# Kernel optimization log

Hardware: AMD Instinct MI355X
Metric: run time of the kernel (lower is better)

## Reference

```python
import jax, jax.numpy as jnp
from jax import lax
import numpy as np
from jax.scipy.ndimage import map_coordinates

SIGMA = 1.0
RADIUS = 3          # from radius=(3,3); kernel size 7
TAU = (2.0, 2.0)
SCALE_FACTORS = (0.5, 1.0)
ITERATIONS = (2, 2)  # production uses (100,100); reduced for tractable reference
EPS = 1e-9
IN_EPS = 1e-5


def gaussian_kernel1d(sigma, radius):
    x = jnp.arange(-radius, radius + 1, dtype=jnp.float32)
    k = jnp.exp(-0.5 * (x / sigma) ** 2)
    return k / jnp.sum(k)


def smooth3d(vf, k):
    # separable depthwise Gaussian over the 3 spatial axes, SAME padding
    C = vf.shape[1]
    for ax in range(3):
        shp = [1, 1, 1]
        shp[ax] = k.shape[0]
        w = jnp.tile(k.reshape(1, 1, *shp), (C, 1, 1, 1, 1))
        vf = lax.conv_general_dilated(vf, w, (1, 1, 1), 'SAME',
                                      dimension_numbers=('NCDHW', 'OIDHW', 'NCDHW'),
                                      feature_group_count=C)
    return vf


def warp(img, vf):
    # img: [1,1,D,H,W], vf: [1,3,D,H,W] displacement in voxel units
    D, H, W = img.shape[2:]
    gz, gy, gx = jnp.meshgrid(jnp.arange(D, dtype=img.dtype),
                              jnp.arange(H, dtype=img.dtype),
                              jnp.arange(W, dtype=img.dtype), indexing='ij')
    coords = [gz + vf[0, 0], gy + vf[0, 1], gx + vf[0, 2]]
    out = map_coordinates(img[0, 0], coords, order=1, mode='nearest')
    return out[None, None]


def demon_forces(warped, fixed, spacing):
    # active demons: gradient of the (warped) moving image
    diff = warped - fixed  # [1,1,D,H,W]
    g = jnp.stack(jnp.gradient(warped[0, 0]), axis=0)[None]  # [1,3,D,H,W]
    g = g / spacing[None, :, None, None, None]
    denom = jnp.sum(g * g, axis=1, keepdims=True) + diff * diff
    return jnp.where(denom > EPS, diff * g / denom, 0.0)


def match_vf(vf, shape):
    # resize displacement field and rescale its magnitude per axis
    old = vf.shape[2:]
    if tuple(old) == tuple(shape):
        return vf
    scale = jnp.array([s1 / s2 for s1, s2 in zip(shape, old)], jnp.float32)
    vf = jax.image.resize(vf, vf.shape[:2] + tuple(shape), method='trilinear')
    return vf * scale[None, :, None, None, None]


def conv3d(x, w):
    return lax.conv_general_dilated(x, w, (1, 1, 1), 'SAME',
                                    dimension_numbers=('NCDHW', 'OIDHW', 'NCDHW'))


def instance_norm(x):
    m = jnp.mean(x, axis=(2, 3, 4), keepdims=True)
    v = jnp.var(x, axis=(2, 3, 4), keepdims=True)
    return (x - m) / jnp.sqrt(v + IN_EPS)


def mish(x):
    return x * jnp.tanh(jax.nn.softplus(x))


def setup_inputs() -> dict:
    key = jax.random.key(0)
    ks = jax.random.split(key, 8)
    D = 96
    image = jax.random.normal(ks[0], (1, 1, D, D, D), jnp.float32)
    moving = jax.random.normal(ks[1], (1, 1, D, D, D), jnp.float32)
    mask = jnp.ones((1, 1, D, D, D), jnp.float32)
    spacing = jnp.ones((3,), jnp.float32)
    w1 = jax.random.normal(ks[2], (32, 5, 3, 3, 3), jnp.float32) * 0.05
    w2 = jax.random.normal(ks[3], (64, 32, 3, 3, 3), jnp.float32) * 0.05
    w3 = jax.random.normal(ks[4], (32, 64, 3, 3, 3), jnp.float32) * 0.05
    w4 = jax.random.normal(ks[5], (3, 32, 3, 3, 3), jnp.float32) * 0.05
    b4 = jnp.zeros((3,), jnp.float32)
    return {'image': image, 'mask': mask, 'moving': moving, 'spacing': spacing,
            'w1': w1, 'w2': w2, 'w3': w3, 'w4': w4, 'b4': b4}


def reference(image, mask, moving, spacing, w1, w2, w3, w4, b4):
    kernel = gaussian_kernel1d(SIGMA, RADIUS)
    full_shape = image.shape[2:]
    vf = None
    for lvl, (sf, n_it) in enumerate(zip(SCALE_FACTORS, ITERATIONS)):
        shp = tuple(int(s * sf) for s in full_shape)
        f = jax.image.resize(image, image.shape[:2] + shp, method='trilinear')
        m = jax.image.resize(mask, mask.shape[:2] + shp, method='nearest')
        mv = jax.image.resize(moving, moving.shape[:2] + shp, method='trilinear')
        if vf is None:
            vf = jnp.zeros((image.shape[0], 3) + shp, jnp.float32)
        else:
            vf = match_vf(vf, shp)
        tau = TAU[lvl]

        def body(i, vf, mv=mv, f=f, m=m, tau=tau):
            warped = warp(mv, vf)
            vf = vf + tau * demon_forces(warped, f, spacing) * m
            return smooth3d(vf, kernel)

        vf = lax.fori_loop(0, n_it, body, vf)

    # the iterative registration runs under torch.no_grad()
    vf = lax.stop_gradient(vf)
    warped_moving = lax.stop_gradient(warp(moving, vf))  # last level is full scale

    # correction CNN: Conv3d/InstanceNorm3d/Mish stack on [vf, image*mask, warped_moving]
    x = jnp.concatenate([vf, image * mask, warped_moving], axis=1)  # [1,5,D,H,W]
    x = mish(instance_norm(conv3d(x, w1)))
    x = mish(instance_norm(conv3d(x, w2)))
    x = mish(instance_norm(conv3d(x, w3)))
    correction = conv3d(x, w4) + b4[None, :, None, None, None]
    corrected_vf = smooth3d(vf + correction, kernel)

    vf = match_vf(vf, full_shape)
    corrected_vf = match_vf(corrected_vf, full_shape)
    corrected_warped_moving = warp(moving, corrected_vf)
    return corrected_warped_moving, corrected_vf, vf
```

## Files before the change

### kernel.cpp

```cpp
#include <hip/hip_runtime.h>
#include <hip/hip_bf16.h>
#include <math.h>

#define DEV __device__ __forceinline__

constexpr int D96 = 96;
constexpr int N96 = D96 * D96 * D96;
constexpr int D48 = 48;
constexpr int N48 = D48 * D48 * D48;

#define GW0 0.3990502796524549f
#define GW1 0.2420362293761143f
#define GW2 0.05400558262251696f
#define GW3 0.004433048175243745f

typedef __attribute__((ext_vector_type(8))) short s16x8;
typedef __attribute__((ext_vector_type(4))) short s16x4;
typedef __attribute__((ext_vector_type(4))) float f32x4;
typedef __attribute__((ext_vector_type(16))) float f32x16;

DEV int clampi(int v, int lo, int hi) { return v < lo ? lo : (v > hi ? hi : v); }

DEV short f2bf(float f) { __hip_bfloat16 h = __float2bfloat16(f); short s; __builtin_memcpy(&s, &h, 2); return s; }
DEV float bf2f(short s) { __hip_bfloat16 h; __builtin_memcpy(&h, &s, 2); return __bfloat162float(h); }

__global__ void k_downsample2x(const float* __restrict__ src, float* __restrict__ dst)
{
    int idx = blockIdx.x * blockDim.x + threadIdx.x;
    if (idx >= N48) return;
    int x = idx % D48, y = (idx / D48) % D48, z = idx / (D48 * D48);

    float wz[4], wy[4], wx[4];
    int jz[4], jy[4], jx[4];
    auto mk = [](int i, float* w, int* j) {
        const float base[4] = {0.125f, 0.375f, 0.375f, 0.125f};
        float s = 0.f;
        #pragma unroll
        for (int t = 0; t < 4; ++t) {
            int jj = 2 * i - 1 + t;
            bool v = (jj >= 0) && (jj < D96);
            j[t] = v ? jj : 0;
            w[t] = v ? base[t] : 0.f;
            s += w[t];
        }
        float inv = 1.f / s;
        #pragma unroll
        for (int t = 0; t < 4; ++t) w[t] *= inv;
    };
    mk(z, wz, jz); mk(y, wy, jy); mk(x, wx, jx);

    float acc = 0.f;
    #pragma unroll
    for (int a = 0; a < 4; ++a) {
        #pragma unroll
        for (int b = 0; b < 4; ++b) {
            float wab = wz[a] * wy[b];
            int rowoff = (jz[a] * D96 + jy[b]) * D96;
            #pragma unroll
            for (int c = 0; c < 4; ++c)
                acc += wab * wx[c] * src[rowoff + jx[c]];
        }
    }
    dst[idx] = acc;
}

__global__ void k_upsample_vf(const float* __restrict__ src, float* __restrict__ dst)
{
    int idx = blockIdx.x * blockDim.x + threadIdx.x;
    if (idx >= 3 * N96) return;
    int c = idx / N96;
    int s = idx - c * N96;
    int x = s % D96, y = (s / D96) % D96, z = s / (D96 * D96);

    auto mk = [](int i, int* j, float* w) {
        int k = i >> 1;
        if ((i & 1) == 0) { j[0] = k - 1; w[0] = 0.25f; j[1] = k; w[1] = 0.75f; }
        else              { j[0] = k;     w[0] = 0.75f; j[1] = k + 1; w[1] = 0.25f; }
        float sum = 0.f;
        #pragma unroll
        for (int t = 0; t < 2; ++t) {
            bool v = (j[t] >= 0) && (j[t] < D48);
            if (!v) { w[t] = 0.f; j[t] = 0; }
            sum += w[t];
        }
        float inv = 1.f / sum;
        w[0] *= inv; w[1] *= inv;
    };
    int jz[2], jy[2], jx[2]; float wz[2], wy[2], wx[2];
    mk(z, jz, wz); mk(y, jy, wy); mk(x, jx, wx);

    const float* p = src + (size_t)c * N48;
    float acc = 0.f;
    #pragma unroll
    for (int a = 0; a < 2; ++a)
        #pragma unroll
        for (int b = 0; b < 2; ++b) {
            float wab = wz[a] * wy[b];
            int rowoff = (jz[a] * D48 + jy[b]) * D48;
            acc += wab * (wx[0] * p[rowoff + jx[0]] + wx[1] * p[rowoff + jx[1]]);
        }
    dst[idx] = 2.f * acc;
}

__global__ void k_warp(const float* __restrict__ img, const float* __restrict__ vf,
                       float* __restrict__ out, int D)
{
    int N = D * D * D;
    int idx = blockIdx.x * blockDim.x + threadIdx.x;
    if (idx >= N) return;
    int x = idx % D, y = (idx / D) % D, z = idx / (D * D);
    float cz = z + vf[idx], cy = y + vf[N + idx], cx = x + vf[2 * N + idx];
    float fz = floorf(cz), fy = floorf(cy), fx = floorf(cx);
    float wz = cz - fz, wy = cy - fy, wx = cx - fx;
    int z0 = clampi((int)fz, 0, D - 1), z1 = clampi((int)fz + 1, 0, D - 1);
    int y0 = clampi((int)fy, 0, D - 1), y1 = clampi((int)fy + 1, 0, D - 1);
    int x0 = clampi((int)fx, 0, D - 1), x1 = clampi((int)fx + 1, 0, D - 1);
    float v000 = img[(z0 * D + y0) * D + x0], v001 = img[(z0 * D + y0) * D + x1];
    float v010 = img[(z0 * D + y1) * D + x0], v011 = img[(z0 * D + y1) * D + x1];
    float v100 = img[(z1 * D + y0) * D + x0], v101 = img[(z1 * D + y0) * D + x1];
    float v110 = img[(z1 * D + y1) * D + x0], v111 = img[(z1 * D + y1) * D + x1];
    float c00 = v000 + wx * (v001 - v000);
    float c01 = v010 + wx * (v011 - v010);
    float c10 = v100 + wx * (v101 - v100);
    float c11 = v110 + wx * (v111 - v110);
    float c0 = c00 + wy * (c01 - c00);
    float c1 = c10 + wy * (c11 - c10);
    out[idx] = c0 + wz * (c1 - c0);
}

__global__ void k_forces(const float* __restrict__ warped, const float* __restrict__ fixed,
                         const float* __restrict__ mask, const float* __restrict__ spacing,
                         float* __restrict__ vf, int D, int maskD, float tau)
{
    int N = D * D * D;
    int idx = blockIdx.x * blockDim.x + threadIdx.x;
    if (idx >= N) return;
    int x = idx % D, y = (idx / D) % D, z = idx / (D * D);
    float w0 = warped[idx];
    float diff = w0 - fixed[idx];
    int sZ = D * D, sY = D;
    float gz = (z == 0) ? warped[idx + sZ] - w0 : (z == D - 1) ? w0 - warped[idx - sZ]
               : 0.5f * (warped[idx + sZ] - warped[idx - sZ]);
    float gy = (y == 0) ? warped[idx + sY] - w0 : (y == D - 1) ? w0 - warped[idx - sY]
               : 0.5f * (warped[idx + sY] - warped[idx - sY]);
    float gx = (x == 0) ? warped[idx + 1] - w0 : (x == D - 1) ? w0 - warped[idx - 1]
               : 0.5f * (warped[idx + 1] - warped[idx - 1]);
    gz /= spacing[0]; gy /= spacing[1]; gx /= spacing[2];
    float denom = gz * gz + gy * gy + gx * gx + diff * diff;
    float m;
    if (D == maskD) m = mask[idx];
    else {
        float r = (float)maskD / (float)D;
        int mz = clampi((int)((z + 0.5f) * r), 0, maskD - 1);
        int my = clampi((int)((y + 0.5f) * r), 0, maskD - 1);
        int mx = clampi((int)((x + 0.5f) * r), 0, maskD - 1);
        m = mask[(mz * maskD + my) * maskD + mx];
    }
    if (denom > 1e-9f) {
        float sc = tau * diff / denom * m;
        vf[idx]         += sc * gz;
        vf[N + idx]     += sc * gy;
        vf[2 * N + idx] += sc * gx;
    }
}

__global__ __launch_bounds__(256, 2)
void k_smooth3(const float* __restrict__ src, float* __restrict__ dst, int D)
{
    __shared__ float B1[10648];
    __shared__ float B2[7744];
    float* B3 = B1;
    int nt = D >> 4;
    int b = blockIdx.x;
    int tx = b % nt, ty = (b / nt) % nt, tz = b / (nt * nt);
    int c = blockIdx.y;
    int N = D * D * D;
    const float* s = src + (size_t)c * N;
    float* d = dst + (size_t)c * N;
    int x0 = tx * 16, y0 = ty * 16, z0 = tz * 16;
    int tid = threadIdx.x;

    for (int l = tid; l < 10648; l += 256) {
        int xx = l % 22, yy = (l / 22) % 22, zz = l / 484;
        int gz = z0 + zz - 3, gy = y0 + yy - 3, gx = x0 + xx - 3;
        float v = 0.f;
        if ((unsigned)gz < (unsigned)D && (unsigned)gy < (unsigned)D && (unsigned)gx < (unsigned)D)
            v = s[((size_t)gz * D + gy) * D + gx];
        B1[l] = v;
    }
    __syncthreads();
    for (int l = tid; l < 16 * 484; l += 256) {
        int xx = l % 22, yy = (l / 22) % 22, zo = l / 484;
        int base = (zo + 3) * 484 + yy * 22 + xx;
        B2[l] = GW0 * B1[base]
              + GW1 * (B1[base - 484] + B1[base + 484])
              + GW2 * (B1[base - 968] + B1[base + 968])
              + GW3 * (B1[base - 1452] + B1[base + 1452]);
    }
    __syncthreads();
    for (int l = tid; l < 16 * 16 * 22; l += 256) {
        int xx = l % 22, yo = (l / 22) % 16, zo = l / 352;
        int base = zo * 484 + (yo + 3) * 22 + xx;
        B3[l] = GW0 * B2[base]
              + GW1 * (B2[base - 22] + B2[base + 22])
              + GW2 * (B2[base - 44] + B2[base + 44])
              + GW3 * (B2[base - 66] + B2[base + 66]);
    }
    __syncthreads();
    for (int l = tid; l < 4096; l += 256) {
        int xo = l % 16, yo = (l / 16) % 16, zo = l / 256;
        int base = zo * 352 + yo * 22 + xo + 3;
        float a = GW0 * B3[base]
                + GW1 * (B3[base - 1] + B3[base + 1])
                + GW2 * (B3[base - 2] + B3[base + 2])
                + GW3 * (B3[base - 3] + B3[base + 3]);
        d[((size_t)(z0 + zo) * D + (y0 + yo)) * D + (x0 + xo)] = a;
    }
}

__global__ void k_pack_cl(const float* __restrict__ vf, const float* __restrict__ image,
                          const float* __restrict__ mask, const float* __restrict__ warped,
                          short* __restrict__ xin8)
{
    int i = blockIdx.x * blockDim.x + threadIdx.x;
    if (i >= N96) return;
    s16x8 v;
    v[0] = f2bf(vf[i]); v[1] = f2bf(vf[N96 + i]); v[2] = f2bf(vf[2 * N96 + i]);
    v[3] = f2bf(image[i] * mask[i]); v[4] = f2bf(warped[i]);
    v[5] = 0; v[6] = 0; v[7] = 0;
    *reinterpret_cast<s16x8*>(&xin8[(size_t)i * 8]) = v;
}

__global__ void k_wreorder_all(const float* __restrict__ w1, const float* __restrict__ w2,
                               const float* __restrict__ w3, const float* __restrict__ w4,
                               short* __restrict__ r1, short* __restrict__ r2,
                               short* __restrict__ r3, short* __restrict__ r4)
{
    int i = blockIdx.x * 256 + threadIdx.x;
    const int S1 = 7168, S2 = 55296, S3 = 55296, S4 = 13824;
    const float* w; short* r; int CIN, CINP, COUT, COUTP;
    int idx = i;
    if (idx < S1)              { w = w1; r = r1; CIN = 5;  CINP = 8;  COUT = 32; COUTP = 32; }
    else if ((idx -= S1) < S2) { w = w2; r = r2; CIN = 32; CINP = 32; COUT = 64; COUTP = 64; }
    else if ((idx -= S2) < S3) { w = w3; r = r3; CIN = 64; CINP = 64; COUT = 32; COUTP = 32; }
    else if ((idx -= S3) < S4) { w = w4; r = r4; CIN = 32; CINP = 32; COUT = 3;  COUTP = 16; }
    else return;
    int j = idx & 7;
    int co = (idx >> 3) % COUTP;
    int kg = idx / (8 * COUTP);
    int k = kg * 8 + j;
    int off = k / CINP, ci = k % CINP;
    float v = 0.f;
    if (co < COUT && off < 27 && ci < CIN)
        v = w[((size_t)co * CIN + ci) * 27 + off];
    r[idx] = f2bf(v);
}

DEV float mishf(float f)
{
    float e = __expf(f);
    float t = 1.f + e;
    float u = t * t + 1.f;
    return f - 2.f * f * __builtin_amdgcn_rcpf(u);
}

__global__ __launch_bounds__(256, 4)
void k_conv1(const short* __restrict__ act, const short* __restrict__ Wr,
             short* __restrict__ outcl, float* __restrict__ part)
{
    constexpr int YH = 6, TN = 3, KS = 14;
    constexpr int TILE_G = 3 * YH * 98;
    __shared__ __align__(16) short tile[TILE_G * 8];
    float* red = (float*)tile;

    int b = blockIdx.x;
    int xcd = b & 7, bidx = b >> 3;
    int zblk = xcd * 12 + bidx / 24;
    int y0 = (bidx % 24) * 4;

    int tid = threadIdx.x;
    int lane = tid & 63, wave = tid >> 6;
    int ln31 = lane & 31, hi = lane >> 5;

    for (int i = tid; i < TILE_G; i += 256) {
        int xi = i % 98, yi = (i / 98) % YH, zi = i / (98 * YH);
        int gz = zblk + zi - 1, gy = y0 + yi - 1, gx = xi - 1;
        s16x8 v = {0, 0, 0, 0, 0, 0, 0, 0};
        if ((unsigned)gz < 96u && (unsigned)gy < 96u && (unsigned)gx < 96u)
            v = *reinterpret_cast<const s16x8*>(&act[(size_t)((gz * 96 + gy) * 96 + gx) * 8]);
        *reinterpret_cast<s16x8*>(&tile[i * 8]) = v;
    }
    __syncthreads();

    f32x16 acc[TN];
    #pragma unroll
    for (int i = 0; i < TN; ++i)
        #pragma unroll
        for (int e = 0; e < 16; ++e) acc[i][e] = 0.f;

    int xb_[TN];
    #pragma unroll
    for (int i = 0; i < TN; ++i) xb_[i] = i * 32 + ln31;

    #pragma unroll
    for (int ks = 0; ks < KS; ++ks) {
        s16x8 a = *reinterpret_cast<const s16x8*>(&Wr[((size_t)(ks * 2 + hi) * 32 + ln31) * 8]);
        int off = ks * 2 + hi; if (off > 26) off = 26;
        int dz = off / 9, r9 = off - dz * 9, dy = r9 / 3, dx = r9 - dy * 3;
        #pragma unroll
        for (int i = 0; i < TN; ++i) {
            int gi = (dz * YH + wave + dy) * 98 + xb_[i] + dx;
            s16x8 bf = *reinterpret_cast<const s16x8*>(&tile[gi * 8]);
            acc[i] = __builtin_amdgcn_mfma_f32_32x32x16_bf16(a, bf, acc[i], 0, 0, 0);
        }
    }

    float st_s[16], st_q[16];
    #pragma unroll
    for (int j = 0; j < 16; ++j) { st_s[j] = 0.f; st_q[j] = 0.f; }
    #pragma unroll
    for (int i = 0; i < TN; ++i)
        #pragma unroll
        for (int e = 0; e < 16; ++e) {
            float v = acc[i][e];
            st_s[e] += v; st_q[e] += v * v;
        }
    #pragma unroll
    for (int j = 0; j < 16; ++j) {
        #pragma unroll
        for (int o = 1; o <= 16; o <<= 1) {
            st_s[j] += __shfl_xor(st_s[j], o);
            st_q[j] += __shfl_xor(st_q[j], o);
        }
    }

    __syncthreads();
    #pragma unroll
    for (int i = 0; i < TN; ++i) {
        int x = xb_[i];
        #pragma unroll
        for (int q = 0; q < 4; ++q) {
            s16x4 pk;
            #pragma unroll
            for (int r = 0; r < 4; ++r) pk[r] = f2bf(acc[i][q * 4 + r]);
            int bo = (((wave * 96 + x) * 32 + q * 8 + hi * 4) * 2) ^ ((x & 3) << 4);
            *reinterpret_cast<s16x4*>((char*)tile + bo) = pk;
        }
    }
    __syncthreads();
    for (int t = tid; t < 4 * 96 * 4; t += 256) {
        int gran = t & 3;
        int x = (t >> 2) % 96;
        int row = t / (4 * 96);
        int bo = (((row * 96 + x) * 32) * 2 + gran * 16) ^ ((x & 3) << 4);
        s16x8 v = *reinterpret_cast<const s16x8*>((char*)tile + bo);
        int vox = ((zblk * 96) + y0 + row) * 96 + x;
        *reinterpret_cast<s16x8*>(&outcl[(size_t)vox * 32 + gran * 8]) = v;
    }

    __syncthreads();
    if (ln31 == 0) {
        int base = (wave * 2 + hi) * 16;
        #pragma unroll
        for (int j = 0; j < 16; ++j) {
            red[(base + j) * 2]     = st_s[j];
            red[(base + j) * 2 + 1] = st_q[j];
        }
    }
    __syncthreads();
    if (tid < 64) {
        int c = tid >> 1, sel = tid & 1;
        int q = (c >> 3) & 3, hic = (c >> 2) & 1, r = c & 3;
        int j = q * 4 + r;
        float v = 0.f;
        #pragma unroll
        for (int w = 0; w < 4; ++w)
            v += red[((w * 2 + hic) * 16 + j) * 2 + sel];
        part[((size_t)c * gridDim.x + blockIdx.x) * 2 + sel] = v;
    }
}

__global__ __launch_bounds__(256, 4)
void k_conv_c2(const short* __restrict__ act, const short* __restrict__ Wr,
               short* __restrict__ outcl, float* __restrict__ part)
{
    constexpr int TN = 3, YH = 6;
    __shared__ __align__(16) short tile[YH * 98 * 32];
    float* red = (float*)tile;

    int bb = blockIdx.x;
    int xcd = bb & 7;
    int ch = (bb >> 3) & 1;
    int idx = bb >> 4;
    int zblk = xcd * 12 + idx / 24;
    int y0 = (idx % 24) * 4;
    int tileid = xcd * 288 + idx;

    int tid = threadIdx.x;
    int lane = tid & 63, wave = tid >> 6;
    int ln31 = lane & 31, hi = lane >> 5;

    int xb_[TN];
    #pragma unroll
    for (int i = 0; i < TN; ++i) xb_[i] = i * 32 + ln31;

    int baddr[TN][3][2];
    #pragma unroll
    for (int i = 0; i < TN; ++i)
        #pragma unroll
        for (int dx = 0; dx < 3; ++dx) {
            int xi = xb_[i] + dx;
            int sw = (xi >> 1) & 3;
            #pragma unroll
            for (int gs = 0; gs < 2; ++gs)
                baddr[i][dx][gs] = ((wave * 98 + xi) * 4 + ((gs * 2 + hi) ^ sw)) * 16;
        }

    f32x16 acc[TN];
    #pragma unroll
    for (int i = 0; i < TN; ++i)
        #pragma unroll
        for (int e = 0; e < 16; ++e) acc[i][e] = 0.f;

    for (int p = 0; p < 3; ++p) {
        int gz = zblk + p - 1;
        __syncthreads();
        #pragma unroll
        for (int it = 0; it < 5; ++it) {
            int i = it * 256 + tid;
            if (i < 1176) {
                int g2 = i & 1, x2 = i >> 1;
                int xi = x2 % 98, yi = x2 / 98;
                int gy = y0 + yi - 1, gx = xi - 1;
                s16x8 v0 = {0, 0, 0, 0, 0, 0, 0, 0}, v1 = v0;
                if ((unsigned)gz < 96u && (unsigned)gy < 96u && (unsigned)gx < 96u) {
                    const short* sp = &act[(size_t)((gz * 96 + gy) * 96 + gx) * 32 + g2 * 16];
                    v0 = *reinterpret_cast<const s16x8*>(sp);
                    v1 = *reinterpret_cast<const s16x8*>(sp + 8);
                }
                int s0 = (g2 * 2) ^ ((xi >> 1) & 3);
                short* dp = &tile[((yi * 98 + xi) << 2) * 8];
                *reinterpret_cast<s16x8*>(&dp[s0 * 8]) = v0;
                *reinterpret_cast<s16x8*>(&dp[(s0 ^ 1) * 8]) = v1;
            }
        }
        __syncthreads();
        int kgbase = p * 36;
        #pragma unroll
        for (int ks = 0; ks < 18; ++ks) {
            constexpr int offt[18] = {0,0,1,1,2,2,3,3,4,4,5,5,6,6,7,7,8,8};
            const int off = offt[ks], gs = ks & 1;
            int kg = kgbase + off * 4 + gs * 2 + hi;
            s16x8 A = *reinterpret_cast<const s16x8*>(
                &Wr[((size_t)kg * 64 + ch * 32 + ln31) * 8]);
            const int dy = off / 3, dx = off % 3;
            #pragma unroll
            for (int i = 0; i < TN; ++i) {
                s16x8 bf = *reinterpret_cast<const s16x8*>(
                    (const char*)tile + baddr[i][dx][gs] + dy * 6272);
                acc[i] = __builtin_amdgcn_mfma_f32_32x32x16_bf16(A, bf, acc[i], 0, 0, 0);
            }
        }
    }

    float st_s[16], st_q[16];
    #pragma unroll
    for (int j = 0; j < 16; ++j) { st_s[j] = 0.f; st_q[j] = 0.f; }
    #pragma unroll
    for (int i = 0; i < TN; ++i)
        #pragma unroll
        for (int e = 0; e < 16; ++e) {
            float v = acc[i][e];
            st_s[e] += v; st_q[e] += v * v;
        }
    #pragma unroll
    for (int j = 0; j < 16; ++j) {
        #pragma unroll
        for (int o = 1; o <= 16; o <<= 1) {
            st_s[j] += __shfl_xor(st_s[j], o);
            st_q[j] += __shfl_xor(st_q[j], o);
        }
    }

    __syncthreads();
    #pragma unroll
    for (int i = 0; i < TN; ++i) {
        int x = xb_[i];
        #pragma unroll
        for (int q = 0; q < 4; ++q) {
            s16x4 pk;
            #pragma unroll
            for (int r = 0; r < 4; ++r) pk[r] = f2bf(acc[i][q * 4 + r]);
            int bo = (((wave * 96 + x) * 32 + q * 8 + hi * 4) * 2) ^ ((x & 3) << 4);
            *reinterpret_cast<s16x4*>((char*)tile + bo) = pk;
        }
    }
    __syncthreads();
    for (int t = tid; t < 4 * 96 * 4; t += 256) {
        int gran = t & 3;
        int x = (t >> 2) % 96;
        int row = t / (4 * 96);
        int bo = (((row * 96 + x) * 32) * 2 + gran * 16) ^ ((x & 3) << 4);
        s16x8 v = *reinterpret_cast<const s16x8*>((char*)tile + bo);
        int vox = ((zblk * 96) + y0 + row) * 96 + x;
        *reinterpret_cast<s16x8*>(&outcl[(size_t)vox * 64 + ch * 32 + gran * 8]) = v;
    }

    __syncthreads();
    if (ln31 == 0) {
        int base = (wave * 2 + hi) * 16;
        #pragma unroll
        for (int j = 0; j < 16; ++j) {
            red[(base + j) * 2]     = st_s[j];
            red[(base + j) * 2 + 1] = st_q[j];
        }
    }
    __syncthreads();
    if (tid < 64) {
        int c = tid >> 1, sel = tid & 1;
        int q = (c >> 3) & 3, hic = (c >> 2) & 1, r = c & 3;
        int j = q * 4 + r;
        float v = 0.f;
        #pragma unroll
        for (int w = 0; w < 4; ++w)
            v += red[((w * 2 + hic) * 16 + j) * 2 + sel];
        part[((size_t)(ch * 32 + c) * 2304 + tileid) * 2 + sel] = v;
    }
}

__global__ __launch_bounds__(256, 4)
void k_conv_c3(const short* __restrict__ act, const short* __restrict__ Wr,
               short* __restrict__ outcl, float* __restrict__ part)
{
    constexpr int YH = 6;
    __shared__ __align__(16) short tile[YH * 98 * 32];
    float* red = (float*)tile;

    int bb = blockIdx.x;
    int xcd = bb & 7;
    int ch = (bb >> 3) & 1;
    int idx = bb >> 4;
    int zblk = xcd * 12 + idx / 24;
    int y0 = (idx % 24) * 4;
    int tileid = xcd * 288 + idx;

    int tid = threadIdx.x;
    int lane = tid & 63, wave = tid >> 6;
    int ln15 = lane & 15, lg = lane >> 4;

    int baddr[6][3];
    #pragma unroll
    for (int i = 0; i < 6; ++i)
        #pragma unroll
        for (int dx = 0; dx < 3; ++dx) {
            int xi = i * 16 + ln15 + dx;
            baddr[i][dx] = ((wave * 98 + xi) * 4 + (lg ^ ((xi >> 1) & 3))) * 16;
        }

    f32x4 acc[6];
    #pragma unroll
    for (int i = 0; i < 6; ++i) acc[i] = {0.f, 0.f, 0.f, 0.f};

    for (int p = 0; p < 3; ++p) {
        int gz = zblk + p - 1;
        for (int h = 0; h < 2; ++h) {
            __syncthreads();
            #pragma unroll
            for (int it = 0; it < 5; ++it) {
                int i = it * 256 + tid;
                if (i < 1176) {
                    int g2 = i & 1, x2 = i >> 1;
                    int xi = x2 % 98, yi = x2 / 98;
                    int gy = y0 + yi - 1, gx = xi - 1;
                    s16x8 v0 = {0, 0, 0, 0, 0, 0, 0, 0}, v1 = v0;
                    if ((unsigned)gz < 96u && (unsigned)gy < 96u && (unsigned)gx < 96u) {
                        const short* sp = &act[(size_t)((gz * 96 + gy) * 96 + gx) * 64
                                               + (h * 4 + g2 * 2) * 8];
                        v0 = *reinterpret_cast<const s16x8*>(sp);
                        v1 = *reinterpret_cast<const s16x8*>(sp + 8);
                    }
                    int s0 = (g2 * 2) ^ ((xi >> 1) & 3);
                    short* dp = &tile[((yi * 98 + xi) << 2) * 8];
                    *reinterpret_cast<s16x8*>(&dp[s0 * 8]) = v0;
                    *reinterpret_cast<s16x8*>(&dp[(s0 ^ 1) * 8]) = v1;
                }
            }
            __syncthreads();
            #pragma unroll
            for (int off = 0; off < 9; ++off) {
                int kg = (p * 9 + off) * 8 + h * 4 + lg;
                s16x8 A = *reinterpret_cast<const s16x8*>(
                    &Wr[((size_t)kg * 32 + ch * 16 + ln15) * 8]);
                const int dy = off / 3, dx = off % 3;
                #pragma unroll
                for (int i = 0; i < 6; ++i) {
                    s16x8 bf = *reinterpret_cast<const s16x8*>(
                        (const char*)tile + baddr[i][dx] + dy * 6272);
                    acc[i] = __builtin_amdgcn_mfma_f32_16x16x32_bf16(A, bf, acc[i], 0, 0, 0);
                }
            }
        }
    }

    float st_s[4], st_q[4];
    #pragma unroll
    for (int j = 0; j < 4; ++j) { st_s[j] = 0.f; st_q[j] = 0.f; }
    #pragma unroll
    for (int i = 0; i < 6; ++i)
        #pragma unroll
        for (int r = 0; r < 4; ++r) {
            float v = acc[i][r];
            st_s[r] += v; st_q[r] += v * v;
        }
    #pragma unroll
    for (int j = 0; j < 4; ++j) {
        #pragma unroll
        for (int o = 1; o <= 8; o <<= 1) {
            st_s[j] += __shfl_xor(st_s[j], o);
            st_q[j] += __shfl_xor(st_q[j], o);
        }
    }

    __syncthreads();
    #pragma unroll
    for (int i = 0; i < 6; ++i) {
        int x = i * 16 + ln15;
        s16x4 pk;
        #pragma unroll
        for (int r = 0; r < 4; ++r) pk[r] = f2bf(acc[i][r]);
        int bo = (((wave * 96 + x) * 16 + lg * 4) * 2) ^ ((x & 3) << 4);
        *reinterpret_cast<s16x4*>((char*)tile + bo) = pk;
    }
    __syncthreads();
    for (int t = tid; t < 4 * 96 * 2; t += 256) {
        int gran = t & 1;
        int x = (t >> 1) % 96;
        int row = t / (2 * 96);
        int bo = (((row * 96 + x) * 16) * 2 + gran * 16) ^ ((x & 3) << 4);
        s16x8 v = *reinterpret_cast<const s16x8*>((char*)tile + bo);
        int vox = ((zblk * 96) + y0 + row) * 96 + x;
        *reinterpret_cast<s16x8*>(&outcl[(size_t)vox * 32 + ch * 16 + gran * 8]) = v;
    }

    __syncthreads();
    if (ln15 == 0) {
        int base = (wave * 4 + lg) * 4;
        #pragma unroll
        for (int j = 0; j < 4; ++j) {
            red[(base + j) * 2]     = st_s[j];
            red[(base + j) * 2 + 1] = st_q[j];
        }
    }
    __syncthreads();
    if (tid < 32) {
        int c = tid >> 1, sel = tid & 1;
        float v = 0.f;
        #pragma unroll
        for (int w = 0; w < 4; ++w)
            v += red[((w * 4 + (c >> 2)) * 4 + (c & 3)) * 2 + sel];
        part[((size_t)(ch * 16 + c) * 2304 + tileid) * 2 + sel] = v;
    }
}

__global__ __launch_bounds__(256, 4)
void k_conv4(const short* __restrict__ act, const short* __restrict__ Wr,
             const float* __restrict__ bias, const float* __restrict__ vf,
             float* __restrict__ corr, float* __restrict__ outvf)
{
    constexpr int YH = 6;
    __shared__ __align__(16) short tile[YH * 98 * 32];

    int b = blockIdx.x;
    int xcd = b & 7, bidx = b >> 3;
    int zblk = xcd * 12 + bidx / 24;
    int y0 = (bidx % 24) * 4;

    int tid = threadIdx.x;
    int lane = tid & 63, wave = tid >> 6;
    int ln15 = lane & 15, lg = lane >> 4;

    int baddr[6][3];
    #pragma unroll
    for (int i = 0; i < 6; ++i)
        #pragma unroll
        for (int dx = 0; dx < 3; ++dx) {
            int xi = i * 16 + ln15 + dx;
            baddr[i][dx] = ((wave * 98 + xi) * 4 + (lg ^ ((xi >> 1) & 3))) * 16;
        }

    f32x4 acc[6];
    #pragma unroll
    for (int i = 0; i < 6; ++i) acc[i] = {0.f, 0.f, 0.f, 0.f};

    for (int p = 0; p < 3; ++p) {
        int gz = zblk + p - 1;
        __syncthreads();
        #pragma unroll
        for (int it = 0; it < 5; ++it) {
            int i = it * 256 + tid;
            if (i < 1176) {
                int g2 = i & 1, x2 = i >> 1;
                int xi = x2 % 98, yi = x2 / 98;
                int gy = y0 + yi - 1, gx = xi - 1;
                s16x8 v0 = {0, 0, 0, 0, 0, 0, 0, 0}, v1 = v0;
                if ((unsigned)gz < 96u && (unsigned)gy < 96u && (unsigned)gx < 96u) {
                    const short* sp = &act[(size_t)((gz * 96 + gy) * 96 + gx) * 32 + g2 * 16];
                    v0 = *reinterpret_cast<const s16x8*>(sp);
                    v1 = *reinterpret_cast<const s16x8*>(sp + 8);
                }
                int s0 = (g2 * 2) ^ ((xi >> 1) & 3);
                short* dp = &tile[((yi * 98 + xi) << 2) * 8];
                *reinterpret_cast<s16x8*>(&dp[s0 * 8]) = v0;
                *reinterpret_cast<s16x8*>(&dp[(s0 ^ 1) * 8]) = v1;
            }
        }
        __syncthreads();
        #pragma unroll
        for (int ks = 0; ks < 9; ++ks) {
            int kg = (p * 9 + ks) * 4 + lg;
            s16x8 a = *reinterpret_cast<const s16x8*>(&Wr[((size_t)kg * 16 + ln15) * 8]);
            const int dy = ks / 3, dx = ks % 3;
            #pragma unroll
            for (int i = 0; i < 6; ++i) {
                s16x8 bf = *reinterpret_cast<const s16x8*>(
                    (const char*)tile + baddr[i][dx] + dy * 6272);
                acc[i] = __builtin_amdgcn_mfma_f32_16x16x32_bf16(a, bf, acc[i], 0, 0, 0);
            }
        }
    }
    if (lg == 0) {
        #pragma unroll
        for (int i = 0; i < 6; ++i) {
            int vox = ((zblk * 96) + y0 + wave) * 96 + i * 16 + ln15;
            #pragma unroll
            for (int r = 0; r < 3; ++r) {
                float v = vf[(size_t)r * N96 + vox];
                corr[(size_t)r * N96 + vox] = acc[i][r] + bias[r] + v;
                outvf[(size_t)r * N96 + vox] = v;
            }
        }
    }
}

template <int C>
__global__ void k_norm_mish_cl(short* __restrict__ x, const float* __restrict__ stats)
{
    constexpr int G8 = C / 8;
    int gt = blockIdx.x * 256 + threadIdx.x;
    int cg = threadIdx.x % G8;
    float mean[8], inv[8];
    #pragma unroll
    for (int j = 0; j < 8; ++j) { mean[j] = stats[2 * (cg * 8 + j)]; inv[j] = stats[2 * (cg * 8 + j) + 1]; }
    const int TGn = N96 * G8;
    int stride = gridDim.x * 256;
    for (int i = gt; i < TGn; i += stride) {
        s16x8 v = *reinterpret_cast<const s16x8*>(&x[(size_t)i * 8]);
        #pragma unroll
        for (int j = 0; j < 8; ++j)
            v[j] = f2bf(mishf((bf2f(v[j]) - mean[j]) * inv[j]));
        *reinterpret_cast<s16x8*>(&x[(size_t)i * 8]) = v;
    }
}

__global__ void k_stats_reduce(const float* __restrict__ part, float* __restrict__ stats,
                               int G, int N)
{
    int c = blockIdx.x;
    int t = threadIdx.x;
    float s = 0.f, s2 = 0.f;
    for (int i = t; i < G; i += blockDim.x) {
        s  += part[((size_t)c * G + i) * 2];
        s2 += part[((size_t)c * G + i) * 2 + 1];
    }
    #pragma unroll
    for (int o = 32; o > 0; o >>= 1) { s += __shfl_down(s, o); s2 += __shfl_down(s2, o); }
    __shared__ float a[4], b[4];
    int lane = t & 63, wid = t >> 6;
    if (lane == 0) { a[wid] = s; b[wid] = s2; }
    __syncthreads();
    if (t == 0) {
        float ss = a[0] + a[1] + a[2] + a[3];
        float qq = b[0] + b[1] + b[2] + b[3];
        float mean = ss / (float)N;
        float var = qq / (float)N - mean * mean;
        stats[2 * c] = mean;
        stats[2 * c + 1] = rsqrtf(var + 1e-5f);
    }
}

extern "C" void kernel_launch(void* const* d_in, const int* in_sizes, int n_in,
                              void* d_out, int out_size, void* d_ws, size_t ws_size,
                              hipStream_t stream)
{
    const float* image   = (const float*)d_in[0];
    const float* mask    = (const float*)d_in[1];
    const float* moving  = (const float*)d_in[2];
    const float* spacing = (const float*)d_in[3];
    const float* w1 = (const float*)d_in[4];
    const float* w2 = (const float*)d_in[5];
    const float* w3 = (const float*)d_in[6];
    const float* w4 = (const float*)d_in[7];
    const float* b4 = (const float*)d_in[8];
    float* out = (float*)d_out;

    char* ws = (char*)d_ws;
    size_t off = 0;
    auto alloc = [&](size_t bytes) -> char* {
        char* p = ws + off;
        off += (bytes + 255) & ~(size_t)255;
        return p;
    };
    float* f48   = (float*)alloc((size_t)N48 * 4);
    float* mv48  = (float*)alloc((size_t)N48 * 4);
    float* vfA48 = (float*)alloc((size_t)3 * N48 * 4);
    float* vfB48 = (float*)alloc((size_t)3 * N48 * 4);
    float* wrp48 = (float*)alloc((size_t)N48 * 4);
    float* vfA96 = (float*)alloc((size_t)3 * N96 * 4);
    float* vfB96 = (float*)alloc((size_t)3 * N96 * 4);
    float* vfC96 = (float*)alloc((size_t)3 * N96 * 4);
    float* wrp96 = (float*)alloc((size_t)N96 * 4);
    short* xin8  = (short*)alloc((size_t)8 * N96 * 2);
    short* y1    = (short*)alloc((size_t)32 * N96 * 2);
    short* y2    = (short*)alloc((size_t)64 * N96 * 2);
    short* wr1   = (short*)alloc((size_t)7168 * 2);
    short* wr2   = (short*)alloc((size_t)55296 * 2);
    short* wr3   = (short*)alloc((size_t)55296 * 2);
    short* wr4   = (short*)alloc((size_t)13824 * 2);
    float* part  = (float*)alloc((size_t)64 * 2304 * 2 * 4);
    float* stats = (float*)alloc((size_t)64 * 2 * 4);

    const int B = 256;
    const int g48  = (N48 + B - 1) / B;
    const int g96  = (N96 + B - 1) / B;
    const int g96c = (3 * N96 + B - 1) / B;

    k_wreorder_all<<<(131584 + 255) / 256, B, 0, stream>>>(w1, w2, w3, w4, wr1, wr2, wr3, wr4);

    k_downsample2x<<<g48, B, 0, stream>>>(image, f48);
    k_downsample2x<<<g48, B, 0, stream>>>(moving, mv48);
    hipMemsetAsync(vfA48, 0, (size_t)3 * N48 * 4, stream);
    float* cur = vfA48; float* oth = vfB48;
    for (int it = 0; it < 2; ++it) {
        k_warp<<<g48, B, 0, stream>>>(mv48, cur, wrp48, D48);
        k_forces<<<g48, B, 0, stream>>>(wrp48, f48, mask, spacing, cur, D48, D96, 2.0f);
        k_smooth3<<<dim3(27, 3), B, 0, stream>>>(cur, oth, D48);
        float* tmp = cur; cur = oth; oth = tmp;
    }

    k_upsample_vf<<<g96c, B, 0, stream>>>(cur, vfA96);
    float* cur9 = vfA96; float* oth9 = vfB96;
    for (int it = 0; it < 2; ++it) {
        k_warp<<<g96, B, 0, stream>>>(moving, cur9, wrp96, D96);
        k_forces<<<g96, B, 0, stream>>>(wrp96, image, mask, spacing, cur9, D96, D96, 2.0f);
        k_smooth3<<<dim3(216, 3), B, 0, stream>>>(cur9, oth9, D96);
        float* tmp = cur9; cur9 = oth9; oth9 = tmp;
    }

    k_warp<<<g96, B, 0, stream>>>(moving, cur9, wrp96, D96);
    k_pack_cl<<<g96, B, 0, stream>>>(cur9, image, mask, wrp96, xin8);

    k_conv1<<<2304, B, 0, stream>>>(xin8, wr1, y1, part);
    k_stats_reduce<<<32, B, 0, stream>>>(part, stats, 2304, N96);
    k_norm_mish_cl<32><<<2048, B, 0, stream>>>(y1, stats);

    k_conv_c2<<<4608, B, 0, stream>>>(y1, wr2, y2, part);
    k_stats_reduce<<<64, B, 0, stream>>>(part, stats, 2304, N96);
    k_norm_mish_cl<64><<<2048, B, 0, stream>>>(y2, stats);

    k_conv_c3<<<4608, B, 0, stream>>>(y2, wr3, y1, part);
    k_stats_reduce<<<32, B, 0, stream>>>(part, stats, 2304, N96);
    k_norm_mish_cl<32><<<2048, B, 0, stream>>>(y1, stats);

    k_conv4<<<2304, B, 0, stream>>>(y1, wr4, b4, cur9, vfC96, out + (size_t)4 * N96);

    k_smooth3<<<dim3(216, 3), B, 0, stream>>>(vfC96, out + N96, D96);

    k_warp<<<g96, B, 0, stream>>>(moving, out + N96, out, D96);
}
```

Measured before the change: 683.5 us.

## Prefetch next z-plane tile into registers while MFMA computes current plane

The three implicit-GEMM conv kernels now issue the global loads for the next input plane (or channel half) into registers before running the MFMA loop on the current LDS tile. After a barrier they write the prefetched data into LDS. This overlaps global memory latency with tensor-core compute, so each stage no longer stalls on its own loads. It costs up to 80 extra VGPRs per thread for the prefetch buffers, which may lower occupancy or cause spills.

```diff
diff --git a/kernel.cpp b/kernel.cpp
--- a/kernel.cpp
+++ b/kernel.cpp
@@ -422,9 +422,8 @@
         #pragma unroll
         for (int e = 0; e < 16; ++e) acc[i][e] = 0.f;
 
-    for (int p = 0; p < 3; ++p) {
-        int gz = zblk + p - 1;
-        __syncthreads();
+    {
+        int gz = zblk - 1;
         #pragma unroll
         for (int it = 0; it < 5; ++it) {
             int i = it * 256 + tid;
@@ -444,7 +443,30 @@
                 *reinterpret_cast<s16x8*>(&dp[(s0 ^ 1) * 8]) = v1;
             }
         }
-        __syncthreads();
+    }
+    __syncthreads();
+
+    for (int p = 0; p < 3; ++p) {
+        s16x8 pre[5][2];
+        if (p < 2) {
+            int gz = zblk + p;
+            #pragma unroll
+            for (int it = 0; it < 5; ++it) {
+                int i = it * 256 + tid;
+                pre[it][0] = (s16x8){0, 0, 0, 0, 0, 0, 0, 0};
+                pre[it][1] = pre[it][0];
+                if (i < 1176) {
+                    int g2 = i & 1, x2 = i >> 1;
+                    int xi = x2 % 98, yi = x2 / 98;
+                    int gy = y0 + yi - 1, gx = xi - 1;
+                    if ((unsigned)gz < 96u && (unsigned)gy < 96u && (unsigned)gx < 96u) {
+                        const short* sp = &act[(size_t)((gz * 96 + gy) * 96 + gx) * 32 + g2 * 16];
+                        pre[it][0] = *reinterpret_cast<const s16x8*>(sp);
+                        pre[it][1] = *reinterpret_cast<const s16x8*>(sp + 8);
+                    }
+                }
+            }
+        }
         int kgbase = p * 36;
         #pragma unroll
         for (int ks = 0; ks < 18; ++ks) {
@@ -460,6 +482,22 @@
                     (const char*)tile + baddr[i][dx][gs] + dy * 6272);
                 acc[i] = __builtin_amdgcn_mfma_f32_32x32x16_bf16(A, bf, acc[i], 0, 0, 0);
             }
+        }
+        __syncthreads();
+        if (p < 2) {
+            #pragma unroll
+            for (int it = 0; it < 5; ++it) {
+                int i = it * 256 + tid;
+                if (i < 1176) {
+                    int g2 = i & 1, x2 = i >> 1;
+                    int xi = x2 % 98, yi = x2 / 98;
+                    int s0 = (g2 * 2) ^ ((xi >> 1) & 3);
+                    short* dp = &tile[((yi * 98 + xi) << 2) * 8];
+                    *reinterpret_cast<s16x8*>(&dp[s0 * 8]) = pre[it][0];
+                    *reinterpret_cast<s16x8*>(&dp[(s0 ^ 1) * 8]) = pre[it][1];
+                }
+            }
+            __syncthreads();
         }
     }
 
@@ -561,44 +599,82 @@
     #pragma unroll
     for (int i = 0; i < 6; ++i) acc[i] = {0.f, 0.f, 0.f, 0.f};
 
-    for (int p = 0; p < 3; ++p) {
-        int gz = zblk + p - 1;
-        for (int h = 0; h < 2; ++h) {
-            __syncthreads();
+    {
+        int gz = zblk - 1;
+        #pragma unroll
+        for (int it = 0; it < 5; ++it) {
+            int i = it * 256 + tid;
+            if (i < 1176) {
+                int g2 = i & 1, x2 = i >> 1;
+                int xi = x2 % 98, yi = x2 / 98;
+                int gy = y0 + yi - 1, gx = xi - 1;
+                s16x8 v0 = {0, 0, 0, 0, 0, 0, 0, 0}, v1 = v0;
+                if ((unsigned)gz < 96u && (unsigned)gy < 96u && (unsigned)gx < 96u) {
+                    const short* sp = &act[(size_t)((gz * 96 + gy) * 96 + gx) * 64 + g2 * 16];
+                    v0 = *reinterpret_cast<const s16x8*>(sp);
+                    v1 = *reinterpret_cast<const s16x8*>(sp + 8);
+                }
+                int s0 = (g2 * 2) ^ ((xi >> 1) & 3);
+                short* dp = &tile[((yi * 98 + xi) << 2) * 8];
+                *reinterpret_cast<s16x8*>(&dp[s0 * 8]) = v0;
+                *reinterpret_cast<s16x8*>(&dp[(s0 ^ 1) * 8]) = v1;
+            }
+        }
+    }
+    __syncthreads();
+
+    for (int ph = 0; ph < 6; ++ph) {
+        s16x8 pre[5][2];
+        if (ph < 5) {
+            int pn = (ph + 1) >> 1, hn = (ph + 1) & 1;
+            int gz = zblk + pn - 1;
+            #pragma unroll
+            for (int it = 0; it < 5; ++it) {
+                int i = it * 256 + tid;
+                pre[it][0] = (s16x8){0, 0, 0, 0, 0, 0, 0, 0};
+                pre[it][1] = pre[it][0];
+                if (i < 1176) {
+                    int g2 = i & 1, x2 = i >> 1;
+                    int xi = x2 % 98, yi = x2 / 98;
+                    int gy = y0 + yi - 1, gx = xi - 1;
+                    if ((unsigned)gz < 96u && (unsigned)gy < 96u && (unsigned)gx < 96u) {
+                        const short* sp = &act[(size_t)((gz * 96 + gy) * 96 + gx) * 64
+                                               + hn * 32 + g2 * 16];
+                        pre[it][0] = *reinterpret_cast<const s16x8*>(sp);
+                        pre[it][1] = *reinterpret_cast<const s16x8*>(sp + 8);
+                    }
+                }
+            }
+        }
+        int p = ph >> 1, h = ph & 1;
+        #pragma unroll
+        for (int off = 0; off < 9; ++off) {
+            int kg = (p * 9 + off) * 8 + h * 4 + lg;
+            s16x8 A = *reinterpret_cast<const s16x8*>(
+                &Wr[((size_t)kg * 32 + ch * 16 + ln15) * 8]);
+            const int dy = off / 3, dx = off % 3;
+            #pragma unroll
+            for (int i = 0; i < 6; ++i) {
+                s16x8 bf = *reinterpret_cast<const s16x8*>(
+                    (const char*)tile + baddr[i][dx] + dy * 6272);
+                acc[i] = __builtin_amdgcn_mfma_f32_16x16x32_bf16(A, bf, acc[i], 0, 0, 0);
+            }
+        }
+        __syncthreads();
+        if (ph < 5) {
             #pragma unroll
             for (int it = 0; it < 5; ++it) {
                 int i = it * 256 + tid;
                 if (i < 1176) {
                     int g2 = i & 1, x2 = i >> 1;
                     int xi = x2 % 98, yi = x2 / 98;
-                    int gy = y0 + yi - 1, gx = xi - 1;
-                    s16x8 v0 = {0, 0, 0, 0, 0, 0, 0, 0}, v1 = v0;
-                    if ((unsigned)gz < 96u && (unsigned)gy < 96u && (unsigned)gx < 96u) {
-                        const short* sp = &act[(size_t)((gz * 96 + gy) * 96 + gx) * 64
-                                               + (h * 4 + g2 * 2) * 8];
-                        v0 = *reinterpret_cast<const s16x8*>(sp);
-                        v1 = *reinterpret_cast<const s16x8*>(sp + 8);
-                    }
                     int s0 = (g2 * 2) ^ ((xi >> 1) & 3);
                     short* dp = &tile[((yi * 98 + xi) << 2) * 8];
-                    *reinterpret_cast<s16x8*>(&dp[s0 * 8]) = v0;
-                    *reinterpret_cast<s16x8*>(&dp[(s0 ^ 1) * 8]) = v1;
+                    *reinterpret_cast<s16x8*>(&dp[s0 * 8]) = pre[it][0];
+                    *reinterpret_cast<s16x8*>(&dp[(s0 ^ 1) * 8]) = pre[it][1];
                 }
             }
             __syncthreads();
-            #pragma unroll
-            for (int off = 0; off < 9; ++off) {
-                int kg = (p * 9 + off) * 8 + h * 4 + lg;
-                s16x8 A = *reinterpret_cast<const s16x8*>(
-                    &Wr[((size_t)kg * 32 + ch * 16 + ln15) * 8]);
-                const int dy = off / 3, dx = off % 3;
-                #pragma unroll
-                for (int i = 0; i < 6; ++i) {
-                    s16x8 bf = *reinterpret_cast<const s16x8*>(
-                        (const char*)tile + baddr[i][dx] + dy * 6272);
-                    acc[i] = __builtin_amdgcn_mfma_f32_16x16x32_bf16(A, bf, acc[i], 0, 0, 0);
-                }
-            }
         }
     }
 
@@ -692,9 +768,8 @@
     #pragma unroll
     for (int i = 0; i < 6; ++i) acc[i] = {0.f, 0.f, 0.f, 0.f};
 
-    for (int p = 0; p < 3; ++p) {
-        int gz = zblk + p - 1;
-        __syncthreads();
+    {
+        int gz = zblk - 1;
         #pragma unroll
         for (int it = 0; it < 5; ++it) {
             int i = it * 256 + tid;
@@ -714,7 +789,30 @@
                 *reinterpret_cast<s16x8*>(&dp[(s0 ^ 1) * 8]) = v1;
             }
         }
-        __syncthreads();
+    }
+    __syncthreads();
+
+    for (int p = 0; p < 3; ++p) {
+        s16x8 pre[5][2];
+        if (p < 2) {
+            int gz = zblk + p;
+            #pragma unroll
+            for (int it = 0; it < 5; ++it) {
+                int i = it * 256 + tid;
+                pre[it][0] = (s16x8){0, 0, 0, 0, 0, 0, 0, 0};
+                pre[it][1] = pre[it][0];
+                if (i < 1176) {
+                    int g2 = i & 1, x2 = i >> 1;
+                    int xi = x2 % 98, yi = x2 / 98;
+                    int gy = y0 + yi - 1, gx = xi - 1;
+                    if ((unsigned)gz < 96u && (unsigned)gy < 96u && (unsigned)gx < 96u) {
+                        const short* sp = &act[(size_t)((gz * 96 + gy) * 96 + gx) * 32 + g2 * 16];
+                        pre[it][0] = *reinterpret_cast<const s16x8*>(sp);
+                        pre[it][1] = *reinterpret_cast<const s16x8*>(sp + 8);
+                    }
+                }
+            }
+        }
         #pragma unroll
         for (int ks = 0; ks < 9; ++ks) {
             int kg = (p * 9 + ks) * 4 + lg;
@@ -726,6 +824,22 @@
                     (const char*)tile + baddr[i][dx] + dy * 6272);
                 acc[i] = __builtin_amdgcn_mfma_f32_16x16x32_bf16(a, bf, acc[i], 0, 0, 0);
             }
+        }
+        __syncthreads();
+        if (p < 2) {
+            #pragma unroll
+            for (int it = 0; it < 5; ++it) {
+                int i = it * 256 + tid;
+                if (i < 1176) {
+                    int g2 = i & 1, x2 = i >> 1;
+                    int xi = x2 % 98, yi = x2 / 98;
+                    int s0 = (g2 * 2) ^ ((xi >> 1) & 3);
+                    short* dp = &tile[((yi * 98 + xi) << 2) * 8];
+                    *reinterpret_cast<s16x8*>(&dp[s0 * 8]) = pre[it][0];
+                    *reinterpret_cast<s16x8*>(&dp[(s0 ^ 1) * 8]) = pre[it][1];
+                }
+            }
+            __syncthreads();
         }
     }
     if (lg == 0) {
```

Measured after the change: 752.2 us. 10.1% more time.
